# Kernel tuning notes

Hardware: AMD Instinct MI355X
Metric: run time of the kernel (lower is better)

The kernel has to match this reference:

```python
import jax, jax.numpy as jnp
import numpy as np

# Graph dimensions (homogeneous node ordering per hetero2homo: [function, input, output])
N_F, N_I, N_O = 2000, 500, 500
N = N_F + N_I + N_O
C = 8                 # hidden channels per function node
H = N_F * C           # total hidden width
B = 256
E_FF, E_IF, E_FO = 40000, 5000, 2000
E = E_FF + E_IF + E_FO
EPS = 1e-5


def _build_graph():
    rng = np.random.default_rng(0)
    src_ff = rng.integers(0, N_F, E_FF)
    dst_ff = rng.integers(0, N_F, E_FF)
    src_if = rng.integers(N_F, N_F + N_I, E_IF)          # input -> function
    dst_if = rng.integers(0, N_F, E_IF)
    src_fo = rng.integers(0, N_F, E_FO)                   # function -> output
    dst_fo = rng.integers(N_F + N_I, N, E_FO)
    src = np.concatenate([src_ff, src_if, src_fo])
    dst = np.concatenate([dst_ff, dst_if, dst_fo])
    edge_index = jnp.asarray(np.stack([src, dst]), dtype=jnp.int32)
    mask = np.zeros(N, dtype=bool)
    mask[N_F + N_I:] = True
    return edge_index, jnp.asarray(mask)


def setup_inputs() -> dict:
    key = jax.random.key(0)
    k_x, k_w1, k_b1, k_w2, k_b2 = jax.random.split(key, 5)
    edge_index, output_node_mask = _build_graph()
    scale = 0.1  # xavier-ish for small fan-in/out
    return {
        "x": jax.random.normal(k_x, (B, N), dtype=jnp.float32),
        "w1": jax.random.normal(k_w1, (E, C), dtype=jnp.float32) * scale,
        "b1": jax.random.normal(k_b1, (H,), dtype=jnp.float32) * 0.01,
        "gamma": jnp.ones((H,), dtype=jnp.float32),
        "beta": jnp.zeros((H,), dtype=jnp.float32),
        "w2": jax.random.normal(k_w2, (E, C), dtype=jnp.float32) * scale,
        "b2": jax.random.normal(k_b2, (E,), dtype=jnp.float32) * 0.01,
        "edge_index": edge_index,
        "output_node_mask": output_node_mask,
        "layers": 10,
    }


def reference(x, w1, b1, gamma, beta, w2, b2, edge_index, output_node_mask, layers):
    src, dst = edge_index[0], edge_index[1]
    # W_in structure: hidden channel k of function node n receives edge e iff dst[e]==n.
    # Edges whose dst is not a function node are structurally absent -> route to dummy segment N_F.
    dst_seg = jnp.where(dst < N_F, dst, N_F)
    # W_out structure: edge e receives hidden channels of function node src[e]; zero otherwise.
    src_is_func = src < N_F
    src_clip = jnp.where(src_is_func, src, 0)

    xe = x[:, src]  # node2edge: (B, E)
    for _ in range(layers):
        # lin_in: sparse (E x H) matmul == per-edge outer product scatter-added onto dst node channels
        contrib = xe.T[:, :, None] * w1[:, None, :]                       # (E, B, C)
        hid = jax.ops.segment_sum(contrib, dst_seg, num_segments=N_F + 1)[:N_F]  # (N_F, B, C)
        h = hid.transpose(1, 0, 2).reshape(B, H) + b1                      # (B, H)
        # layer norm then nonlin (norm_first=True)
        mu = h.mean(-1, keepdims=True)
        var = h.var(-1, keepdims=True)
        h = (h - mu) * jax.lax.rsqrt(var + EPS) * gamma + beta
        h = jax.nn.elu(h)
        # lin_out: sparse (H x E) matmul == gather src-node channels, dot with per-edge weights
        hn = h.reshape(B, N_F, C)
        out_e = jnp.einsum('bec,ec->be', hn[:, src_clip, :], w2)
        out_e = jnp.where(src_is_func[None, :], out_e, 0.0) + b2[None, :]
        xe = xe + out_e                                                    # residual
    xe = xe / layers
    # edge2node: scatter-add edge features onto output nodes only
    xm = jnp.where(output_node_mask[dst][None, :], xe, 0.0)
    out = jax.ops.segment_sum(xm.T, dst, num_segments=output_node_mask.shape[0]).T  # (B, N)
    return out
```

## Files before the change

kernel.cpp:

```cpp
#include <hip/hip_runtime.h>
#include <cmath>
#include <cstdint>

#define N_F    2000
#define N_I    500
#define N_O    500
#define N_ALL  3000
#define C      8
#define H      16000
#define B      256
#define E_FF   40000
#define E_IF   5000
#define E_FO   2000
#define E_ALL  47000
#define LAYERS 10
#define EPSF   1e-5f
#define RED    32

static __device__ __forceinline__ unsigned short f2bf(float f) {
    unsigned int u = __float_as_uint(f);
    unsigned int r = (u + 0x7FFFu + ((u >> 16) & 1u)) >> 16;
    return (unsigned short)r;
}
static __device__ __forceinline__ float bf2f(unsigned short h) {
    return __uint_as_float(((unsigned int)h) << 16);
}


__global__ void k_zero_cnt(int* cntA, int* cntB, int* cntC, int* cntD) {
    int tid = threadIdx.x;
    for (int i = tid; i < N_F; i += 1024) { cntA[i] = 0; cntB[i] = 0; cntC[i] = 0; }
    for (int i = tid; i < N_O; i += 1024) cntD[i] = 0;
}

__global__ void k_count(const int* __restrict__ src, const int* __restrict__ dst,
                        int* cntA, int* cntB, int* cntC, int* cntD) {
    int e = blockIdx.x * 256 + threadIdx.x;
    if (e >= E_ALL) return;
    int s = src[e], d = dst[e];
    if (e < E_FF)             { atomicAdd(&cntA[d], 1); atomicAdd(&cntB[d], 1); atomicAdd(&cntC[s], 1); }
    else if (e < E_FF + E_IF) { atomicAdd(&cntA[d], 1); }
    else                      { atomicAdd(&cntD[d - (N_F + N_I)], 1); }
}

__global__ void k_scan(const int* cntA, const int* cntB, const int* cntC, const int* cntD,
                       int* rsA, int* rsB2, int* rsC, int* rsD,
                       int* curA, int* curB, int* curC, int* curD) {
    const int* cnt; int* rs; int* cur; int len;
    if      (blockIdx.x == 0) { cnt = cntA; rs = rsA;  cur = curA; len = N_F; }
    else if (blockIdx.x == 1) { cnt = cntB; rs = rsB2; cur = curB; len = N_F; }
    else if (blockIdx.x == 2) { cnt = cntC; rs = rsC;  cur = curC; len = N_F; }
    else                      { cnt = cntD; rs = rsD;  cur = curD; len = N_O; }
    __shared__ int buf[1024];
    __shared__ int carry;
    int tid = threadIdx.x;
    if (tid == 0) carry = 0;
    __syncthreads();
    for (int base0 = 0; base0 < len; base0 += 1024) {
        int i = base0 + tid;
        int v = (i < len) ? cnt[i] : 0;
        buf[tid] = v;
        __syncthreads();
        for (int off = 1; off < 1024; off <<= 1) {
            int t = (tid >= off) ? buf[tid - off] : 0;
            __syncthreads();
            buf[tid] += t;
            __syncthreads();
        }
        int excl = carry + buf[tid] - v;
        if (i < len) { rs[i] = excl; cur[i] = excl; }
        int tot = buf[1023];
        __syncthreads();
        if (tid == 0) carry += tot;
        __syncthreads();
    }
    if (tid == 0) rs[len] = carry;
}

__global__ void k_fill(const int* __restrict__ src, const int* __restrict__ dst,
                       int* curA, int* curC, int* curD,
                       int* eidA, int* eidC, int* eidD) {
    int e = blockIdx.x * 256 + threadIdx.x;
    if (e >= E_ALL) return;
    int s = src[e], d = dst[e];
    if (e < E_FF) {
        int a = atomicAdd(&curA[d], 1); eidA[a] = e;
        int p = atomicAdd(&curC[s], 1); eidC[p] = e;
    } else if (e < E_FF + E_IF) {
        int a = atomicAdd(&curA[d], 1); eidA[a] = e;
    } else {
        int k = atomicAdd(&curD[d - (N_F + N_I)], 1); eidD[k] = e;
    }
}

__global__ void k_wsort(const int* __restrict__ rsA, int* eidA,
                        const int* __restrict__ rsC, int* eidC,
                        const int* __restrict__ rsD, int* eidD) {
    int w = blockIdx.x * 4 + (threadIdx.x >> 6);
    int lane = threadIdx.x & 63;
    const int* rs; int* eid; int n;
    if      (w < 2000) { rs = rsA; eid = eidA; n = w; }
    else if (w < 4000) { rs = rsC; eid = eidC; n = w - 2000; }
    else if (w < 4500) { rs = rsD; eid = eidD; n = w - 4000; }
    else return;
    int beg = rs[n], end = rs[n + 1], len = end - beg;
    if (len <= 1) return;
    if (len <= 64) {
        int v = (lane < len) ? eid[beg + lane] : 0x7fffffff;
        int rank = 0;
        for (int j = 0; j < 64; ++j) {
            int o = __shfl(v, j, 64);
            rank += (o < v) ? 1 : 0;
        }
        if (lane < len) eid[beg + rank] = v;
    } else if (lane == 0) {
        for (int i = beg + 1; i < end; ++i) {
            int key = eid[i];
            int j = i - 1;
            while (j >= beg && eid[j] > key) { eid[j + 1] = eid[j]; --j; }
            eid[j + 1] = key;
        }
    }
}

__global__ void k_posB(const int* __restrict__ rsA, const int* __restrict__ eidA,
                       const int* __restrict__ cntB, const int* __restrict__ rsB2,
                       const float* __restrict__ w1, int* posB, float* jw1) {
    int w = blockIdx.x * 4 + (threadIdx.x >> 6);
    int lane = threadIdx.x & 63;
    if (w >= N_F) return;
    int a0 = rsA[w], j0 = rsB2[w], m = cntB[w];
    const float4* w14 = (const float4*)w1;
    float4* jw14 = (float4*)jw1;
    for (int k = lane; k < m; k += 64) {
        int e = eidA[a0 + k];
        int j = j0 + k;
        posB[e] = j;
        jw14[j * 2]     = w14[e * 2];
        jw14[j * 2 + 1] = w14[e * 2 + 1];
    }
}

__global__ void k_posC(const int* __restrict__ eidC, const int* __restrict__ posB,
                       const float* __restrict__ w2, int* jposC, float* w2C) {
    int p = blockIdx.x * 256 + threadIdx.x;
    if (p >= E_FF) return;
    int e = eidC[p];
    jposC[p] = posB[e];
    float4 u0 = ((const float4*)w2)[e * 2], u1 = ((const float4*)w2)[e * 2 + 1];
    ((float4*)w2C)[p * 2]     = u0;
    ((float4*)w2C)[p * 2 + 1] = u1;
}


__global__ void k_xT(const float* __restrict__ x, float* __restrict__ xT) {
    __shared__ float t[32][33];
    int tx = threadIdx.x, ty = threadIdx.y;
    int n = blockIdx.x * 32 + tx, b = blockIdx.y * 32 + ty;
    if (n < N_ALL) t[ty][tx] = x[b * N_ALL + n];
    __syncthreads();
    int n2 = blockIdx.x * 32 + ty, b2 = blockIdx.y * 32 + tx;
    if (n2 < N_ALL) xT[n2 * B + b2] = t[tx][ty];
}

__global__ void k_base(const float* __restrict__ xT, const float* __restrict__ w1,
                       const float* __restrict__ b1, const float* __restrict__ b2,
                       const int* __restrict__ rsA, const int* __restrict__ eidA,
                       const int* __restrict__ srcv,
                       unsigned short* __restrict__ baseG, float* __restrict__ bbG) {
    int n = blockIdx.x, tid = threadIdx.x;
    int beg = rsA[n], end = rsA[n + 1];
    float acc[C] = {0.f,0.f,0.f,0.f,0.f,0.f,0.f,0.f};
    float bba[C] = {0.f,0.f,0.f,0.f,0.f,0.f,0.f,0.f};
    const float4* w14 = (const float4*)w1;
    for (int a = beg; a < end; ++a) {
        int e = eidA[a];
        float xv = xT[srcv[e] * B + tid];
        float bv = b2[e];
        float4 u0 = w14[e * 2], u1 = w14[e * 2 + 1];
        acc[0] += u0.x * xv; acc[1] += u0.y * xv; acc[2] += u0.z * xv; acc[3] += u0.w * xv;
        acc[4] += u1.x * xv; acc[5] += u1.y * xv; acc[6] += u1.z * xv; acc[7] += u1.w * xv;
        bba[0] += u0.x * bv; bba[1] += u0.y * bv; bba[2] += u0.z * bv; bba[3] += u0.w * bv;
        bba[4] += u1.x * bv; bba[5] += u1.y * bv; bba[6] += u1.z * bv; bba[7] += u1.w * bv;
    }
    #pragma unroll
    for (int c = 0; c < C; ++c) baseG[(n * C + c) * B + tid] = f2bf(acc[c] + b1[n * C + c]);
    if (tid == 0) {
        #pragma unroll
        for (int c = 0; c < C; ++c) bbG[n * C + c] = bba[c];
    }
}


__global__ __launch_bounds__(256) void f_hidstat(
    const unsigned short* __restrict__ baseG, const float* __restrict__ bbG,
    const float* __restrict__ jw1, const unsigned short* __restrict__ qbf,
    const int* __restrict__ rsB2,
    unsigned short* __restrict__ hidbf, float* __restrict__ bp, int t) {
    int n = blockIdx.x, tid = threadIdx.x;
    const float4* jw14 = (const float4*)jw1;
    float tf = (float)t;
    float hid[C];
    #pragma unroll
    for (int c = 0; c < C; ++c)
        hid[c] = bf2f(baseG[(n * C + c) * B + tid]) + tf * bbG[n * C + c];
    if (t > 0) {
        int beg = rsB2[n], end = rsB2[n + 1];
        for (int j = beg; j < end; ++j) {
            float qv = bf2f(qbf[j * B + tid]);
            float4 u0 = jw14[j * 2], u1 = jw14[j * 2 + 1];
            hid[0] += u0.x * qv; hid[1] += u0.y * qv; hid[2] += u0.z * qv; hid[3] += u0.w * qv;
            hid[4] += u1.x * qv; hid[5] += u1.y * qv; hid[6] += u1.z * qv; hid[7] += u1.w * qv;
        }
    }
    float s1 = 0.f, s2 = 0.f;
    #pragma unroll
    for (int c = 0; c < C; ++c) {
        hidbf[(n * C + c) * B + tid] = f2bf(hid[c]);
        s1 += hid[c]; s2 += hid[c] * hid[c];
    }
    bp[(n * 2 + 0) * B + tid] = s1;
    bp[(n * 2 + 1) * B + tid] = s2;
}

__global__ __launch_bounds__(256) void f_red(const float* __restrict__ bp, float* __restrict__ p2) {
    int blk = blockIdx.x, tid = threadIdx.x;
    float a1 = 0.f, a2 = 0.f;
    for (int i = blk; i < N_F; i += RED) {
        a1 += bp[(i * 2 + 0) * B + tid];
        a2 += bp[(i * 2 + 1) * B + tid];
    }
    p2[(blk * 2 + 0) * B + tid] = a1;
    p2[(blk * 2 + 1) * B + tid] = a2;
}

__global__ __launch_bounds__(256) void f_upd(
    const unsigned short* __restrict__ hidbf, const float* __restrict__ p2,
    const float* __restrict__ gamma, const float* __restrict__ beta,
    const float* __restrict__ w2C, const int* __restrict__ jposC,
    const int* __restrict__ rsC,
    unsigned short* __restrict__ Sg, unsigned short* __restrict__ qbf, int t) {
    int n = blockIdx.x, tid = threadIdx.x;
    const float4* w24 = (const float4*)w2C;
    float S1 = 0.f, S2 = 0.f;
    #pragma unroll
    for (int k = 0; k < RED; ++k) {
        S1 += p2[(k * 2 + 0) * B + tid];
        S2 += p2[(k * 2 + 1) * B + tid];
    }
    float mu  = S1 * (1.0f / H);
    float var = S2 * (1.0f / H) - mu * mu;
    float rsq = rsqrtf(var + EPSF);
    float Sn[C];
    #pragma unroll
    for (int c = 0; c < C; ++c) {
        float v = bf2f(hidbf[(n * C + c) * B + tid]);
        v = (v - mu) * rsq * gamma[n * C + c] + beta[n * C + c];
        v = (v > 0.f) ? v : expm1f(v);
        Sn[c] = (t == 0) ? v : (bf2f(Sg[(n * C + c) * B + tid]) + v);
    }
    #pragma unroll
    for (int c = 0; c < C; ++c) Sg[(n * C + c) * B + tid] = f2bf(Sn[c]);
    if (t < LAYERS - 1) {
        int beg = rsC[n], end = rsC[n + 1];
        for (int p = beg; p < end; ++p) {
            int j = jposC[p];
            float4 u0 = w24[p * 2], u1 = w24[p * 2 + 1];
            float qv = u0.x * Sn[0] + u0.y * Sn[1] + u0.z * Sn[2] + u0.w * Sn[3]
                     + u1.x * Sn[4] + u1.y * Sn[5] + u1.z * Sn[6] + u1.w * Sn[7];
            qbf[j * B + tid] = f2bf(qv);
        }
    }
}


__global__ void f_zero_out(float* __restrict__ out) {
    int i = blockIdx.x * 256 + threadIdx.x;
    ((float4*)out)[i] = make_float4(0.f, 0.f, 0.f, 0.f);
}

__global__ void f_out(const float* __restrict__ xT, const unsigned short* __restrict__ Sg,
                      const int* __restrict__ rsD, const int* __restrict__ eidD,
                      const int* __restrict__ srcv, const float* __restrict__ w2,
                      const float* __restrict__ b2, float* __restrict__ out) {
    int o = blockIdx.x, tid = threadIdx.x;
    const float4* w24 = (const float4*)w2;
    float acc = 0.f;
    int beg = rsD[o], end = rsD[o + 1];
    for (int k = beg; k < end; ++k) {
        int e = eidD[k];
        int s = srcv[e];
        float4 u0 = w24[e * 2], u1 = w24[e * 2 + 1];
        float dot = u0.x * bf2f(Sg[(s * C + 0) * B + tid]) + u0.y * bf2f(Sg[(s * C + 1) * B + tid])
                  + u0.z * bf2f(Sg[(s * C + 2) * B + tid]) + u0.w * bf2f(Sg[(s * C + 3) * B + tid])
                  + u1.x * bf2f(Sg[(s * C + 4) * B + tid]) + u1.y * bf2f(Sg[(s * C + 5) * B + tid])
                  + u1.z * bf2f(Sg[(s * C + 6) * B + tid]) + u1.w * bf2f(Sg[(s * C + 7) * B + tid]);
        acc += xT[s * B + tid] + dot + (float)LAYERS * b2[e];
    }
    out[tid * N_ALL + (N_F + N_I + o)] = acc * (1.0f / LAYERS);
}


static inline char* alignup(char* p) { return (char*)(((uintptr_t)p + 255) & ~(uintptr_t)255); }

extern "C" void kernel_launch(void* const* d_in, const int* in_sizes, int n_in,
                              void* d_out, int out_size, void* d_ws, size_t ws_size,
                              hipStream_t stream) {
    const float* x     = (const float*)d_in[0];
    const float* w1    = (const float*)d_in[1];
    const float* b1    = (const float*)d_in[2];
    const float* gamma = (const float*)d_in[3];
    const float* beta  = (const float*)d_in[4];
    const float* w2    = (const float*)d_in[5];
    const float* b2    = (const float*)d_in[6];
    const int*   ei    = (const int*)d_in[7];
    const int* srcv = ei;
    const int* dstv = ei + E_ALL;
    float* out = (float*)d_out;

    char* p = (char*)d_ws;
    unsigned short* qbf   = (unsigned short*)p; p += (size_t)E_FF * B * 2; p = alignup(p);
    unsigned short* hidbf = (unsigned short*)p; p += (size_t)H * B * 2;    p = alignup(p);
    unsigned short* Sg    = (unsigned short*)p; p += (size_t)H * B * 2;    p = alignup(p);
    unsigned short* baseG = (unsigned short*)p; p += (size_t)H * B * 2;    p = alignup(p);
    float* xT    = (float*)p; p += (size_t)N_ALL * B * 4;    p = alignup(p);
    float* bp    = (float*)p; p += (size_t)N_F * 2 * B * 4;  p = alignup(p);
    float* p2    = (float*)p; p += (size_t)RED * 2 * B * 4;  p = alignup(p);
    float* bbG   = (float*)p; p += (size_t)N_F * C * 4;      p = alignup(p);
    float* jw1   = (float*)p; p += (size_t)E_FF * C * 4;     p = alignup(p);
    float* w2C   = (float*)p; p += (size_t)E_FF * C * 4;     p = alignup(p);
    int* posB  = (int*)p; p += (size_t)E_FF * 4;  p = alignup(p);
    int* jposC = (int*)p; p += (size_t)E_FF * 4;  p = alignup(p);
    int* cntA = (int*)p; p += N_F * 4;        p = alignup(p);
    int* cntB = (int*)p; p += N_F * 4;        p = alignup(p);
    int* cntC = (int*)p; p += N_F * 4;        p = alignup(p);
    int* cntD = (int*)p; p += N_O * 4;        p = alignup(p);
    int* curA = (int*)p; p += N_F * 4;        p = alignup(p);
    int* curB = (int*)p; p += N_F * 4;        p = alignup(p);
    int* curC = (int*)p; p += N_F * 4;        p = alignup(p);
    int* curD = (int*)p; p += N_O * 4;        p = alignup(p);
    int* rsA  = (int*)p; p += (N_F + 1) * 4;  p = alignup(p);
    int* rsB2 = (int*)p; p += (N_F + 1) * 4;  p = alignup(p);
    int* rsC  = (int*)p; p += (N_F + 1) * 4;  p = alignup(p);
    int* rsD  = (int*)p; p += (N_O + 1) * 4;  p = alignup(p);
    int* eidA = (int*)p; p += (size_t)(E_FF + E_IF) * 4; p = alignup(p);
    int* eidC = (int*)p; p += (size_t)E_FF * 4; p = alignup(p);
    int* eidD = (int*)p; p += (size_t)E_FO * 4; p = alignup(p);

    hipLaunchKernelGGL(k_zero_cnt, dim3(1), dim3(1024), 0, stream, cntA, cntB, cntC, cntD);
    hipLaunchKernelGGL(k_count, dim3((E_ALL + 255) / 256), dim3(256), 0, stream,
                       srcv, dstv, cntA, cntB, cntC, cntD);
    hipLaunchKernelGGL(k_scan, dim3(4), dim3(1024), 0, stream,
                       cntA, cntB, cntC, cntD, rsA, rsB2, rsC, rsD, curA, curB, curC, curD);
    hipLaunchKernelGGL(k_fill, dim3((E_ALL + 255) / 256), dim3(256), 0, stream,
                       srcv, dstv, curA, curC, curD, eidA, eidC, eidD);
    hipLaunchKernelGGL(k_wsort, dim3(1125), dim3(256), 0, stream,
                       rsA, eidA, rsC, eidC, rsD, eidD);
    hipLaunchKernelGGL(k_posB, dim3((N_F + 3) / 4), dim3(256), 0, stream,
                       rsA, eidA, cntB, rsB2, w1, posB, jw1);
    hipLaunchKernelGGL(k_posC, dim3((E_FF + 255) / 256), dim3(256), 0, stream,
                       eidC, posB, w2, jposC, w2C);
    hipLaunchKernelGGL(k_xT, dim3((N_ALL + 31) / 32, B / 32), dim3(32, 32), 0, stream, x, xT);
    hipLaunchKernelGGL(k_base, dim3(N_F), dim3(256), 0, stream,
                       xT, w1, b1, b2, rsA, eidA, srcv, baseG, bbG);

    hipLaunchKernelGGL(f_zero_out, dim3(750), dim3(256), 0, stream, out);
    for (int t = 0; t < LAYERS; ++t) {
        hipLaunchKernelGGL(f_hidstat, dim3(N_F), dim3(256), 0, stream,
                           baseG, bbG, jw1, qbf, rsB2, hidbf, bp, t);
        hipLaunchKernelGGL(f_red, dim3(RED), dim3(256), 0, stream, bp, p2);
        hipLaunchKernelGGL(f_upd, dim3(N_F), dim3(256), 0, stream,
                           hidbf, p2, gamma, beta, w2C, jposC, rsC, Sg, qbf, t);
    }
    hipLaunchKernelGGL(f_out, dim3(N_O), dim3(256), 0, stream,
                       xT, Sg, rsD, eidD, srcv, w2, b2, out);
}
```

Baseline: 717.1 us.

## Map one wavefront per node with four batch columns per lane

k_base, f_hidstat and f_upd now give each 64-lane wavefront its own function node, and each lane handles four batch columns. Loads and stores become ushort4/float4 vectors, and the per-edge weight loads are reused across four columns. The grid shrinks to a quarter as many blocks. This trades more registers per thread and less parallelism (500 blocks) for fewer redundant scalar weight and index loads and wider memory transactions.

```diff
diff --git a/kernel.cpp b/kernel.cpp
--- a/kernel.cpp
+++ b/kernel.cpp
@@ -163,29 +163,47 @@
     if (n2 < N_ALL) xT[n2 * B + b2] = t[tx][ty];
 }
 
-__global__ void k_base(const float* __restrict__ xT, const float* __restrict__ w1,
-                       const float* __restrict__ b1, const float* __restrict__ b2,
-                       const int* __restrict__ rsA, const int* __restrict__ eidA,
-                       const int* __restrict__ srcv,
-                       unsigned short* __restrict__ baseG, float* __restrict__ bbG) {
-    int n = blockIdx.x, tid = threadIdx.x;
+__global__ __launch_bounds__(256) void k_base(
+    const float* __restrict__ xT, const float* __restrict__ w1,
+    const float* __restrict__ b1, const float* __restrict__ b2,
+    const int* __restrict__ rsA, const int* __restrict__ eidA,
+    const int* __restrict__ srcv,
+    unsigned short* __restrict__ baseG, float* __restrict__ bbG) {
+    int wv = threadIdx.x >> 6, lane = threadIdx.x & 63;
+    int n = blockIdx.x * 4 + wv;
+    int col = lane * 4;
     int beg = rsA[n], end = rsA[n + 1];
-    float acc[C] = {0.f,0.f,0.f,0.f,0.f,0.f,0.f,0.f};
-    float bba[C] = {0.f,0.f,0.f,0.f,0.f,0.f,0.f,0.f};
+    float acc[C][4];
+    float bba[C];
+    #pragma unroll
+    for (int c = 0; c < C; ++c) {
+        acc[c][0] = acc[c][1] = acc[c][2] = acc[c][3] = 0.f;
+        bba[c] = 0.f;
+    }
     const float4* w14 = (const float4*)w1;
     for (int a = beg; a < end; ++a) {
         int e = eidA[a];
-        float xv = xT[srcv[e] * B + tid];
+        int s = srcv[e];
+        float4 xv = *(const float4*)&xT[s * B + col];
         float bv = b2[e];
         float4 u0 = w14[e * 2], u1 = w14[e * 2 + 1];
-        acc[0] += u0.x * xv; acc[1] += u0.y * xv; acc[2] += u0.z * xv; acc[3] += u0.w * xv;
-        acc[4] += u1.x * xv; acc[5] += u1.y * xv; acc[6] += u1.z * xv; acc[7] += u1.w * xv;
-        bba[0] += u0.x * bv; bba[1] += u0.y * bv; bba[2] += u0.z * bv; bba[3] += u0.w * bv;
-        bba[4] += u1.x * bv; bba[5] += u1.y * bv; bba[6] += u1.z * bv; bba[7] += u1.w * bv;
-    }
-    #pragma unroll
-    for (int c = 0; c < C; ++c) baseG[(n * C + c) * B + tid] = f2bf(acc[c] + b1[n * C + c]);
-    if (tid == 0) {
+        float w[8] = {u0.x, u0.y, u0.z, u0.w, u1.x, u1.y, u1.z, u1.w};
+        #pragma unroll
+        for (int c = 0; c < C; ++c) {
+            acc[c][0] += w[c] * xv.x; acc[c][1] += w[c] * xv.y;
+            acc[c][2] += w[c] * xv.z; acc[c][3] += w[c] * xv.w;
+            bba[c] += w[c] * bv;
+        }
+    }
+    #pragma unroll
+    for (int c = 0; c < C; ++c) {
+        float b1v = b1[n * C + c];
+        ushort4 o;
+        o.x = f2bf(acc[c][0] + b1v); o.y = f2bf(acc[c][1] + b1v);
+        o.z = f2bf(acc[c][2] + b1v); o.w = f2bf(acc[c][3] + b1v);
+        *(ushort4*)&baseG[(n * C + c) * B + col] = o;
+    }
+    if (lane == 0) {
         #pragma unroll
         for (int c = 0; c < C; ++c) bbG[n * C + c] = bba[c];
     }
@@ -197,30 +215,45 @@
     const float* __restrict__ jw1, const unsigned short* __restrict__ qbf,
     const int* __restrict__ rsB2,
     unsigned short* __restrict__ hidbf, float* __restrict__ bp, int t) {
-    int n = blockIdx.x, tid = threadIdx.x;
+    int wv = threadIdx.x >> 6, lane = threadIdx.x & 63;
+    int n = blockIdx.x * 4 + wv;
+    int col = lane * 4;
     const float4* jw14 = (const float4*)jw1;
     float tf = (float)t;
-    float hid[C];
-    #pragma unroll
-    for (int c = 0; c < C; ++c)
-        hid[c] = bf2f(baseG[(n * C + c) * B + tid]) + tf * bbG[n * C + c];
+    float hid[C][4];
+    #pragma unroll
+    for (int c = 0; c < C; ++c) {
+        ushort4 bv = *(const ushort4*)&baseG[(n * C + c) * B + col];
+        float bb = tf * bbG[n * C + c];
+        hid[c][0] = bf2f(bv.x) + bb; hid[c][1] = bf2f(bv.y) + bb;
+        hid[c][2] = bf2f(bv.z) + bb; hid[c][3] = bf2f(bv.w) + bb;
+    }
     if (t > 0) {
         int beg = rsB2[n], end = rsB2[n + 1];
         for (int j = beg; j < end; ++j) {
-            float qv = bf2f(qbf[j * B + tid]);
+            ushort4 qv = *(const ushort4*)&qbf[j * B + col];
+            float q0 = bf2f(qv.x), q1 = bf2f(qv.y), q2 = bf2f(qv.z), q3 = bf2f(qv.w);
             float4 u0 = jw14[j * 2], u1 = jw14[j * 2 + 1];
-            hid[0] += u0.x * qv; hid[1] += u0.y * qv; hid[2] += u0.z * qv; hid[3] += u0.w * qv;
-            hid[4] += u1.x * qv; hid[5] += u1.y * qv; hid[6] += u1.z * qv; hid[7] += u1.w * qv;
-        }
-    }
-    float s1 = 0.f, s2 = 0.f;
+            float w[8] = {u0.x, u0.y, u0.z, u0.w, u1.x, u1.y, u1.z, u1.w};
+            #pragma unroll
+            for (int c = 0; c < C; ++c) {
+                hid[c][0] += w[c] * q0; hid[c][1] += w[c] * q1;
+                hid[c][2] += w[c] * q2; hid[c][3] += w[c] * q3;
+            }
+        }
+    }
+    float s1[4] = {0.f, 0.f, 0.f, 0.f}, s2[4] = {0.f, 0.f, 0.f, 0.f};
     #pragma unroll
     for (int c = 0; c < C; ++c) {
-        hidbf[(n * C + c) * B + tid] = f2bf(hid[c]);
-        s1 += hid[c]; s2 += hid[c] * hid[c];
-    }
-    bp[(n * 2 + 0) * B + tid] = s1;
-    bp[(n * 2 + 1) * B + tid] = s2;
+        ushort4 o;
+        o.x = f2bf(hid[c][0]); o.y = f2bf(hid[c][1]);
+        o.z = f2bf(hid[c][2]); o.w = f2bf(hid[c][3]);
+        *(ushort4*)&hidbf[(n * C + c) * B + col] = o;
+        #pragma unroll
+        for (int k = 0; k < 4; ++k) { s1[k] += hid[c][k]; s2[k] += hid[c][k] * hid[c][k]; }
+    }
+    *(float4*)&bp[(n * 2 + 0) * B + col] = make_float4(s1[0], s1[1], s1[2], s1[3]);
+    *(float4*)&bp[(n * 2 + 1) * B + col] = make_float4(s2[0], s2[1], s2[2], s2[3]);
 }
 
 __global__ __launch_bounds__(256) void f_red(const float* __restrict__ bp, float* __restrict__ p2) {
@@ -240,35 +273,62 @@
     const float* __restrict__ w2C, const int* __restrict__ jposC,
     const int* __restrict__ rsC,
     unsigned short* __restrict__ Sg, unsigned short* __restrict__ qbf, int t) {
-    int n = blockIdx.x, tid = threadIdx.x;
+    int wv = threadIdx.x >> 6, lane = threadIdx.x & 63;
+    int n = blockIdx.x * 4 + wv;
+    int col = lane * 4;
     const float4* w24 = (const float4*)w2C;
-    float S1 = 0.f, S2 = 0.f;
+    float S1[4] = {0.f, 0.f, 0.f, 0.f}, S2[4] = {0.f, 0.f, 0.f, 0.f};
     #pragma unroll
     for (int k = 0; k < RED; ++k) {
-        S1 += p2[(k * 2 + 0) * B + tid];
-        S2 += p2[(k * 2 + 1) * B + tid];
-    }
-    float mu  = S1 * (1.0f / H);
-    float var = S2 * (1.0f / H) - mu * mu;
-    float rsq = rsqrtf(var + EPSF);
-    float Sn[C];
+        float4 a = *(const float4*)&p2[(k * 2 + 0) * B + col];
+        float4 b = *(const float4*)&p2[(k * 2 + 1) * B + col];
+        S1[0] += a.x; S1[1] += a.y; S1[2] += a.z; S1[3] += a.w;
+        S2[0] += b.x; S2[1] += b.y; S2[2] += b.z; S2[3] += b.w;
+    }
+    float mu[4], rsq[4];
+    #pragma unroll
+    for (int k = 0; k < 4; ++k) {
+        mu[k]  = S1[k] * (1.0f / H);
+        float var = S2[k] * (1.0f / H) - mu[k] * mu[k];
+        rsq[k] = rsqrtf(var + EPSF);
+    }
+    float Sn[C][4];
     #pragma unroll
     for (int c = 0; c < C; ++c) {
-        float v = bf2f(hidbf[(n * C + c) * B + tid]);
-        v = (v - mu) * rsq * gamma[n * C + c] + beta[n * C + c];
-        v = (v > 0.f) ? v : expm1f(v);
-        Sn[c] = (t == 0) ? v : (bf2f(Sg[(n * C + c) * B + tid]) + v);
-    }
-    #pragma unroll
-    for (int c = 0; c < C; ++c) Sg[(n * C + c) * B + tid] = f2bf(Sn[c]);
+        ushort4 hv = *(const ushort4*)&hidbf[(n * C + c) * B + col];
+        float g = gamma[n * C + c], be = beta[n * C + c];
+        float h[4] = {bf2f(hv.x), bf2f(hv.y), bf2f(hv.z), bf2f(hv.w)};
+        float sv[4] = {0.f, 0.f, 0.f, 0.f};
+        if (t > 0) {
+            ushort4 s4 = *(const ushort4*)&Sg[(n * C + c) * B + col];
+            sv[0] = bf2f(s4.x); sv[1] = bf2f(s4.y); sv[2] = bf2f(s4.z); sv[3] = bf2f(s4.w);
+        }
+        #pragma unroll
+        for (int k = 0; k < 4; ++k) {
+            float v = (h[k] - mu[k]) * rsq[k] * g + be;
+            v = (v > 0.f) ? v : expm1f(v);
+            Sn[c][k] = (t == 0) ? v : (sv[k] + v);
+        }
+        ushort4 o;
+        o.x = f2bf(Sn[c][0]); o.y = f2bf(Sn[c][1]);
+        o.z = f2bf(Sn[c][2]); o.w = f2bf(Sn[c][3]);
+        *(ushort4*)&Sg[(n * C + c) * B + col] = o;
+    }
     if (t < LAYERS - 1) {
         int beg = rsC[n], end = rsC[n + 1];
         for (int p = beg; p < end; ++p) {
             int j = jposC[p];
             float4 u0 = w24[p * 2], u1 = w24[p * 2 + 1];
-            float qv = u0.x * Sn[0] + u0.y * Sn[1] + u0.z * Sn[2] + u0.w * Sn[3]
-                     + u1.x * Sn[4] + u1.y * Sn[5] + u1.z * Sn[6] + u1.w * Sn[7];
-            qbf[j * B + tid] = f2bf(qv);
+            float w[8] = {u0.x, u0.y, u0.z, u0.w, u1.x, u1.y, u1.z, u1.w};
+            float qv[4] = {0.f, 0.f, 0.f, 0.f};
+            #pragma unroll
+            for (int c = 0; c < C; ++c) {
+                qv[0] += w[c] * Sn[c][0]; qv[1] += w[c] * Sn[c][1];
+                qv[2] += w[c] * Sn[c][2]; qv[3] += w[c] * Sn[c][3];
+            }
+            ushort4 o;
+            o.x = f2bf(qv[0]); o.y = f2bf(qv[1]); o.z = f2bf(qv[2]); o.w = f2bf(qv[3]);
+            *(ushort4*)&qbf[j * B + col] = o;
         }
     }
 }
@@ -361,15 +421,15 @@
     hipLaunchKernelGGL(k_posC, dim3((E_FF + 255) / 256), dim3(256), 0, stream,
                        eidC, posB, w2, jposC, w2C);
     hipLaunchKernelGGL(k_xT, dim3((N_ALL + 31) / 32, B / 32), dim3(32, 32), 0, stream, x, xT);
-    hipLaunchKernelGGL(k_base, dim3(N_F), dim3(256), 0, stream,
+    hipLaunchKernelGGL(k_base, dim3(N_F / 4), dim3(256), 0, stream,
                        xT, w1, b1, b2, rsA, eidA, srcv, baseG, bbG);
 
     hipLaunchKernelGGL(f_zero_out, dim3(750), dim3(256), 0, stream, out);
     for (int t = 0; t < LAYERS; ++t) {
-        hipLaunchKernelGGL(f_hidstat, dim3(N_F), dim3(256), 0, stream,
+        hipLaunchKernelGGL(f_hidstat, dim3(N_F / 4), dim3(256), 0, stream,
                            baseG, bbG, jw1, qbf, rsB2, hidbf, bp, t);
         hipLaunchKernelGGL(f_red, dim3(RED), dim3(256), 0, stream, bp, p2);
-        hipLaunchKernelGGL(f_upd, dim3(N_F), dim3(256), 0, stream,
+        hipLaunchKernelGGL(f_upd, dim3(N_F / 4), dim3(256), 0, stream,
                            hidbf, p2, gamma, beta, w2C, jposC, rsC, Sg, qbf, t);
     }
     hipLaunchKernelGGL(f_out, dim3(N_O), dim3(256), 0, stream,
```

Measured after the change: 826.4 us. 1.15x slower.
